# Kernel optimization log

Hardware: AMD Instinct MI355X
Metric: run time of the kernel (lower is better)

## Reference

```python
import jax, jax.numpy as jnp
import numpy as np
import math

RATIO = 2
KSIZE = 12  # int(6 * ratio // 2) * 2 for ratio = 2
LRELU_SLOPE = 0.1


def _kaiser_sinc_filter1d(cutoff, half_width, ksize):
    """Replicates alias_free_torch.filter.kaiser_sinc_filter1d (numpy, host-side)."""
    even = (ksize % 2 == 0)
    half = ksize // 2
    delta_f = 4.0 * half_width
    A = 2.285 * (half - 1) * math.pi * delta_f + 7.95
    if A > 50.0:
        beta = 0.1102 * (A - 8.7)
    elif A >= 21.0:
        beta = 0.5842 * (A - 21.0) ** 0.4 + 0.07886 * (A - 21.0)
    else:
        beta = 0.0
    win = np.kaiser(ksize, beta)  # == torch.kaiser_window(ksize, periodic=False)
    if even:
        time = np.arange(-half, half) + 0.5
    else:
        time = np.arange(ksize) - half
    filt = 2.0 * cutoff * win * np.sinc(2.0 * cutoff * time)
    filt = filt / filt.sum()
    return filt.astype(np.float32)


def setup_inputs() -> dict:
    key = jax.random.key(0)
    x = jax.random.normal(key, (8, 128, 32768), dtype=jnp.float32)
    up_f = jnp.asarray(_kaiser_sinc_filter1d(0.5 / RATIO, 0.6 / RATIO, KSIZE))
    dn_f = jnp.asarray(_kaiser_sinc_filter1d(0.5 / RATIO, 0.6 / RATIO, KSIZE))
    return {"x": x, "up_filter": up_f, "down_filter": dn_f}


def _depthwise_conv1d(x, filt, stride, lhs_dilation, pad):
    # x: (B, C, L); same 1-tap-bank filter applied per channel -> fold C into batch
    B, C, L = x.shape
    lhs = x.reshape(B * C, 1, L)
    rhs = filt.reshape(1, 1, -1)
    out = jax.lax.conv_general_dilated(
        lhs, rhs,
        window_strides=(stride,),
        padding=[pad],
        lhs_dilation=(lhs_dilation,),
        dimension_numbers=("NCH", "OIH", "NCH"),
    )
    return out.reshape(B, C, -1)


def reference(x, up_filter, down_filter):
    K, r = KSIZE, RATIO
    # ---- UpSample1d: replicate-pad, conv_transpose (stride=r), trim ----
    pad = K // r - 1                         # 5
    pad_left = pad * r + (K - r) // 2        # 15
    pad_right = pad * r + (K - r + 1) // 2   # 15
    xp = jnp.pad(x, ((0, 0), (0, 0), (pad, pad)), mode="edge")
    # conv_transpose == lhs-dilated full conv; kaiser-sinc filter is symmetric,
    # so no kernel flip needed
    up = r * _depthwise_conv1d(xp, up_filter, stride=1, lhs_dilation=r,
                               pad=(K - 1, K - 1))
    up = up[..., pad_left: up.shape[-1] - pad_right]  # (B, C, r*T)
    # ---- elementwise activation: LeakyReLU(0.1) ----
    act = jnp.where(up >= 0, up, LRELU_SLOPE * up)
    # ---- DownSample1d: LowPassFilter1d with replicate pad, stride=r ----
    dl, dr = K // 2 - 1, K // 2              # even kernel: (5, 6)
    ap = jnp.pad(act, ((0, 0), (0, 0), (dl, dr)), mode="edge")
    out = _depthwise_conv1d(ap, down_filter, stride=r, lhs_dilation=1,
                            pad=(0, 0))      # (B, C, T)
    return out
```

## Files before the change

### kernel.cpp

```cpp
#include <hip/hip_runtime.h>


#define LROW   32768
#define OPT    16
#define BLOCK  256
#define TILE   (OPT * BLOCK)
#define KS     12
#define SLOPE  0.1f

typedef float f32x4 __attribute__((ext_vector_type(4)));

__global__ __launch_bounds__(BLOCK) void aa_act_kernel(
    const float* __restrict__ x,
    const float* __restrict__ upf,
    const float* __restrict__ dnf,
    float* __restrict__ out)
{
    const int tid = threadIdx.x;
    const int t   = blockIdx.x * TILE + OPT * tid;
    const size_t row = blockIdx.y;
    const float* __restrict__ xrow = x + row * (size_t)LROW;
    float* __restrict__ orow       = out + row * (size_t)LROW;

    float fu[KS], fd[KS];
#pragma unroll
    for (int k = 0; k < KS; ++k) {
        fu[k] = 2.0f * upf[k];
        fd[k] = dnf[k];
    }

    const int base_g = t - 8;
    float xv[32];
    if (base_g >= 0 && base_g + 32 <= LROW) {
        const f32x4* __restrict__ src = reinterpret_cast<const f32x4*>(xrow + base_g);
#pragma unroll
        for (int q = 0; q < 8; ++q) {
            f32x4 w = src[q];
            xv[4*q+0] = w.x; xv[4*q+1] = w.y; xv[4*q+2] = w.z; xv[4*q+3] = w.w;
        }
    } else {
#pragma unroll
        for (int m = 0; m < 32; ++m) {
            int g = base_g + m;
            g = g < 0 ? 0 : (g >= LROW ? LROW - 1 : g);
            xv[m] = xrow[g];
        }
    }

    float a[42];
#pragma unroll
    for (int d = -2; d <= 18; ++d) {
        float v = 0.0f;
#pragma unroll
        for (int j = 0; j < 6; ++j) v = fmaf(fu[2*j], xv[d + 5 + j], v);
        a[2*d + 5] = v >= 0.0f ? v : SLOPE * v;
    }
#pragma unroll
    for (int d = -3; d <= 17; ++d) {
        float v = 0.0f;
#pragma unroll
        for (int j = 0; j < 6; ++j) v = fmaf(fu[2*j + 1], xv[d + 6 + j], v);
        a[2*d + 6] = v >= 0.0f ? v : SLOPE * v;
    }

    if (t == 0) {
        a[4] = a[5]; a[3] = a[5]; a[2] = a[5]; a[1] = a[5]; a[0] = a[5];
    }
    if (t == LROW - OPT) {
        a[37] = a[36]; a[38] = a[36]; a[39] = a[36]; a[40] = a[36]; a[41] = a[36];
    }

    float o[OPT];
#pragma unroll
    for (int m = 0; m < OPT; ++m) {
        float acc = 0.0f;
#pragma unroll
        for (int k = 0; k < KS; ++k) acc = fmaf(fd[k], a[2*m + k], acc);
        o[m] = acc;
    }

    f32x4* po = reinterpret_cast<f32x4*>(orow + t);
#pragma unroll
    for (int q = 0; q < 4; ++q) {
        po[q] = (f32x4){ o[4*q+0], o[4*q+1], o[4*q+2], o[4*q+3] };
    }
}

extern "C" void kernel_launch(void* const* d_in, const int* in_sizes, int n_in,
                              void* d_out, int out_size, void* d_ws, size_t ws_size,
                              hipStream_t stream) {
    const float* x   = (const float*)d_in[0];
    const float* upf = (const float*)d_in[1];
    const float* dnf = (const float*)d_in[2];
    float* out = (float*)d_out;

    const int rows = in_sizes[0] / LROW;
    dim3 grid(LROW / TILE, rows);
    aa_act_kernel<<<grid, dim3(BLOCK), 0, stream>>>(x, upf, dnf, out);
}
```

Measured before the change: 242.0 us.

## Shrink per-thread output to 4 and process two tiles per thread

```diff
diff --git a/kernel.cpp b/kernel.cpp
--- a/kernel.cpp
+++ b/kernel.cpp
@@ -1,14 +1,73 @@
 #include <hip/hip_runtime.h>
 
 
-#define LROW   32768
-#define OPT    16
-#define BLOCK  256
-#define TILE   (OPT * BLOCK)
-#define KS     12
-#define SLOPE  0.1f
+#define LROW  32768
+#define OPT   4
+#define BLOCK 256
+#define TILE  (OPT * BLOCK)
+#define TPR   (LROW / TILE)
+#define NITER 2
+#define GX    (TPR / NITER)
+#define KS    12
+#define SLOPE 0.1f
 
 typedef float f32x4 __attribute__((ext_vector_type(4)));
+
+__device__ __forceinline__ void load_win(float xv[20], const float* __restrict__ xrow, int t)
+{
+    const int base = t - 8;
+    if (base >= 0 && base + 20 <= LROW) {
+        const f32x4* __restrict__ src = reinterpret_cast<const f32x4*>(xrow + base);
+#pragma unroll
+        for (int q = 0; q < 5; ++q) {
+            f32x4 w = src[q];
+            xv[4*q+0] = w.x; xv[4*q+1] = w.y; xv[4*q+2] = w.z; xv[4*q+3] = w.w;
+        }
+    } else {
+#pragma unroll
+        for (int m = 0; m < 20; ++m) {
+            int g = base + m;
+            g = g < 0 ? 0 : (g >= LROW ? LROW - 1 : g);
+            xv[m] = xrow[g];
+        }
+    }
+}
+
+__device__ __forceinline__ void compute_store(const float xv[20],
+                                              const float fu[KS], const float fd[KS],
+                                              float* __restrict__ orow, int t)
+{
+    float a[18];
+#pragma unroll
+    for (int i = 0; i < 9; ++i) {
+        float vo = 0.0f, ve = 0.0f;
+#pragma unroll
+        for (int j = 0; j < 6; ++j) {
+            const float xx = xv[i + 3 + j];
+            vo = fmaf(fu[2*j + 1], xx, vo);
+            ve = fmaf(fu[2*j],     xx, ve);
+        }
+        a[2*i]     = fmaxf(vo, SLOPE * vo);
+        a[2*i + 1] = fmaxf(ve, SLOPE * ve);
+    }
+
+    if (t == 0) {
+        a[0] = a[5]; a[1] = a[5]; a[2] = a[5]; a[3] = a[5]; a[4] = a[5];
+    }
+    if (t == LROW - OPT) {
+        a[13] = a[12]; a[14] = a[12]; a[15] = a[12]; a[16] = a[12]; a[17] = a[12];
+    }
+
+    float o[OPT];
+#pragma unroll
+    for (int m = 0; m < OPT; ++m) {
+        float acc = 0.0f;
+#pragma unroll
+        for (int k = 0; k < KS; ++k) acc = fmaf(fd[k], a[2*m + k], acc);
+        o[m] = 2.0f * acc;
+    }
+    *reinterpret_cast<f32x4*>(orow + t) = (f32x4){ o[0], o[1], o[2], o[3] };
+}
 
 __global__ __launch_bounds__(BLOCK) void aa_act_kernel(
     const float* __restrict__ x,
@@ -17,73 +76,24 @@
     float* __restrict__ out)
 {
     const int tid = threadIdx.x;
-    const int t   = blockIdx.x * TILE + OPT * tid;
+    const int bx  = blockIdx.x;
     const size_t row = blockIdx.y;
     const float* __restrict__ xrow = x + row * (size_t)LROW;
     float* __restrict__ orow       = out + row * (size_t)LROW;
 
     float fu[KS], fd[KS];
 #pragma unroll
-    for (int k = 0; k < KS; ++k) {
-        fu[k] = 2.0f * upf[k];
-        fd[k] = dnf[k];
-    }
+    for (int k = 0; k < KS; ++k) { fu[k] = upf[k]; fd[k] = dnf[k]; }
 
-    const int base_g = t - 8;
-    float xv[32];
-    if (base_g >= 0 && base_g + 32 <= LROW) {
-        const f32x4* __restrict__ src = reinterpret_cast<const f32x4*>(xrow + base_g);
-#pragma unroll
-        for (int q = 0; q < 8; ++q) {
-            f32x4 w = src[q];
-            xv[4*q+0] = w.x; xv[4*q+1] = w.y; xv[4*q+2] = w.z; xv[4*q+3] = w.w;
-        }
-    } else {
-#pragma unroll
-        for (int m = 0; m < 32; ++m) {
-            int g = base_g + m;
-            g = g < 0 ? 0 : (g >= LROW ? LROW - 1 : g);
-            xv[m] = xrow[g];
-        }
-    }
+    const int tA = bx * TILE + OPT * tid;
+    const int tB = (bx + GX) * TILE + OPT * tid;
 
-    float a[42];
-#pragma unroll
-    for (int d = -2; d <= 18; ++d) {
-        float v = 0.0f;
-#pragma unroll
-        for (int j = 0; j < 6; ++j) v = fmaf(fu[2*j], xv[d + 5 + j], v);
-        a[2*d + 5] = v >= 0.0f ? v : SLOPE * v;
-    }
-#pragma unroll
-    for (int d = -3; d <= 17; ++d) {
-        float v = 0.0f;
-#pragma unroll
-        for (int j = 0; j < 6; ++j) v = fmaf(fu[2*j + 1], xv[d + 6 + j], v);
-        a[2*d + 6] = v >= 0.0f ? v : SLOPE * v;
-    }
+    float xvA[20], xvB[20];
+    load_win(xvA, xrow, tA);
+    load_win(xvB, xrow, tB);
 
-    if (t == 0) {
-        a[4] = a[5]; a[3] = a[5]; a[2] = a[5]; a[1] = a[5]; a[0] = a[5];
-    }
-    if (t == LROW - OPT) {
-        a[37] = a[36]; a[38] = a[36]; a[39] = a[36]; a[40] = a[36]; a[41] = a[36];
-    }
-
-    float o[OPT];
-#pragma unroll
-    for (int m = 0; m < OPT; ++m) {
-        float acc = 0.0f;
-#pragma unroll
-        for (int k = 0; k < KS; ++k) acc = fmaf(fd[k], a[2*m + k], acc);
-        o[m] = acc;
-    }
-
-    f32x4* po = reinterpret_cast<f32x4*>(orow + t);
-#pragma unroll
-    for (int q = 0; q < 4; ++q) {
-        po[q] = (f32x4){ o[4*q+0], o[4*q+1], o[4*q+2], o[4*q+3] };
-    }
+    compute_store(xvA, fu, fd, orow, tA);
+    compute_store(xvB, fu, fd, orow, tB);
 }
 
 extern "C" void kernel_launch(void* const* d_in, const int* in_sizes, int n_in,
@@ -95,6 +105,6 @@
     float* out = (float*)d_out;
 
     const int rows = in_sizes[0] / LROW;
-    dim3 grid(LROW / TILE, rows);
+    dim3 grid(GX, rows);
     aa_act_kernel<<<grid, dim3(BLOCK), 0, stream>>>(x, upf, dnf, out);
 }
```

Measured after the change: 231.3 us. 4.4% less time.
